# Kernel optimization log

Hardware: AMD Instinct MI355X
Metric: run time of the kernel (lower is better)

## Reference

```python
import jax, jax.numpy as jnp
import numpy as np

KS, STRIDE, PAD, GROUPS = 7, 1, 3, 8


def setup_inputs() -> dict:
    key = jax.random.key(0)
    ks = jax.random.split(key, 6)
    B, C, H, W = 4, 128, 64, 64
    O = 128
    rel_size = O // GROUPS // 2  # 8
    return {
        "x": jax.random.normal(ks[0], (B, C, H, W), jnp.float32),
        "wq": jax.random.normal(ks[1], (O, C), jnp.float32) * 0.05,
        "wk": jax.random.normal(ks[2], (O, C), jnp.float32) * 0.05,
        "wv": jax.random.normal(ks[3], (O, C), jnp.float32) * 0.05,
        "rel_x": jax.random.normal(ks[4], (rel_size, KS), jnp.float32),
        "rel_y": jax.random.normal(ks[5], (O // GROUPS - rel_size, KS), jnp.float32),
    }


def _patches(a, fH, fW):
    # a: [B, C, pH, pW] -> [B, C, fH, fW, KS, KS] (overlapping windows, like torch unfold)
    cols = []
    for ki in range(KS):
        rows = []
        for kj in range(KS):
            rows.append(a[:, :, ki:ki + (fH - 1) * STRIDE + 1:STRIDE,
                             kj:kj + (fW - 1) * STRIDE + 1:STRIDE])
        cols.append(jnp.stack(rows, axis=-1))  # last axis = l (W-kernel)
    return jnp.stack(cols, axis=-2)            # second-to-last = k (H-kernel)


def reference(x, wq, wk, wv, rel_x, rel_y):
    B, C, H, W = x.shape
    O = wq.shape[0]
    rel_size = rel_x.shape[0]
    xp = jnp.pad(x, ((0, 0), (0, 0), (PAD, PAD), (PAD, PAD)))
    pH, pW = H + 2 * PAD, W + 2 * PAD
    fH, fW = (pH - KS) // STRIDE + 1, (pW - KS) // STRIDE + 1
    # 1x1 convs
    q = jnp.einsum('oc,bchw->bohw', wq, xp)
    k = jnp.einsum('oc,bchw->bohw', wk, xp)
    v = jnp.einsum('oc,bchw->bohw', wv, xp)
    h0 = (KS - 1) // 2
    win_q = q[:, :, h0:pH - KS // 2:STRIDE, h0:pW - KS // 2:STRIDE]  # [B,O,fH,fW]
    win_q_b = win_q.reshape(B, GROUPS, O // GROUPS, fH, fW)
    qx = win_q_b[:, :, :rel_size]
    qy = win_q_b[:, :, rel_size:]
    bias_x = jnp.einsum('bgxhw,xk->bhwk', qx, rel_x)  # varies along l (W-kernel)
    bias_y = jnp.einsum('bgyhw,yk->bhwk', qy, rel_y)  # varies along k (H-kernel)
    win_k = _patches(k, fH, fW)  # [B,O,fH,fW,KS,KS]
    win_v = _patches(v, fH, fW)
    logits = jnp.einsum('bchw,bchwkl->bhwkl', win_q, win_k)
    logits = logits + bias_x[:, :, :, None, :] + bias_y[:, :, :, :, None]
    attn = jax.nn.softmax(logits.reshape(B, fH, fW, KS * KS), axis=-1)
    attn = attn.reshape(B, fH, fW, KS, KS)
    out = jnp.einsum('bhwkl,bchwkl->bchw', attn, win_v)  # [B,O,fH,fW]
    return out
```

## Files before the change

### kernel.cpp

```cpp
#include <hip/hip_runtime.h>

typedef __fp16 half8_t __attribute__((ext_vector_type(8)));
typedef float  f4_t    __attribute__((ext_vector_type(4)));

__device__ __forceinline__ unsigned pk(float a, float b) {
    return __builtin_bit_cast(unsigned, __builtin_amdgcn_cvt_pkrtz(a, b));
}

__global__ __launch_bounds__(256, 4) void qkv_fused(
    const float* __restrict__ x, const float* __restrict__ wq,
    const float* __restrict__ wk, const float* __restrict__ wv,
    const float* __restrict__ relx, const float* __restrict__ rely,
    unsigned* __restrict__ qf, unsigned* __restrict__ kf,
    unsigned* __restrict__ vf, float* __restrict__ biasG)
{
    __shared__ __fp16 Af[2048 * 8];
    __shared__ float  uB[4][320];
    __shared__ float  relsQ[120];

    const int tid = threadIdx.x, wvn = tid >> 6, lane = tid & 63;
    const int mtx = blockIdx.x >> 8;
    const int tg  = blockIdx.x & 255;
    const float* wsrc = (mtx == 0) ? wq : (mtx == 1 ? wk : wv);
    unsigned*    dst  = (mtx == 0) ? qf : (mtx == 1 ? kf : vf);

    if (tid < 120)
        relsQ[tid] = (tid < 56) ? relx[tid] : (tid < 112 ? rely[tid - 56] : 0.f);

#pragma unroll
    for (int s = 0; s < 8; ++s) {
        const int it = s * 256 + tid;
        const int l = it & 63, ck = (it >> 6) & 3, ot = it >> 8;
        const float* wr = wsrc + (size_t)(ot * 16 + (l & 15)) * 128 + ck * 32 + (l >> 4) * 8;
        const float4 w0 = *(const float4*)wr;
        const float4 w1 = *(const float4*)(wr + 4);
        unsigned* d = (unsigned*)&Af[it * 8];
        d[0] = pk(w0.x, w0.y); d[1] = pk(w0.z, w0.w);
        d[2] = pk(w1.x, w1.y); d[3] = pk(w1.z, w1.w);
    }

    const int t = tg * 4 + wvn;
    const int m = lane & 15, quad = lane >> 4;
    const int p0 = t * 16, b = p0 >> 12, hw = p0 & 4095;
    const float* xb = x + (size_t)b * (128 * 4096) + hw + m;
    half8_t B[4];
#pragma unroll
    for (int ck = 0; ck < 4; ++ck) {
        float f[8];
#pragma unroll
        for (int j = 0; j < 8; ++j) f[j] = xb[(size_t)(ck * 32 + quad * 8 + j) * 4096];
        unsigned* d = (unsigned*)&B[ck];
        d[0] = pk(f[0], f[1]); d[1] = pk(f[2], f[3]);
        d[2] = pk(f[4], f[5]); d[3] = pk(f[6], f[7]);
    }
    __syncthreads();

    float* tl = uB[wvn];
    float s0 = 0.f, s1 = 0.f, s2 = 0.f, s3 = 0.f;
#pragma unroll
    for (int og = 0; og < 4; ++og) {
#pragma unroll
        for (int ot = 0; ot < 2; ++ot) {
            const int otile = og * 2 + ot;
            f4_t acc = {0.f, 0.f, 0.f, 0.f};
#pragma unroll
            for (int ck = 0; ck < 4; ++ck) {
                const half8_t A = *(const half8_t*)&Af[((otile * 4 + ck) * 64 + lane) * 8];
                acc = __builtin_amdgcn_mfma_f32_16x16x32_f16(A, B[ck], acc, 0, 0, 0);
            }
            if (mtx == 0) { s0 += acc[0]; s1 += acc[1]; s2 += acc[2]; s3 += acc[3]; }
            const int c2l = ot * 8 + quad * 2;
            tl[m * 17 + c2l]     = __builtin_bit_cast(float, pk(acc[0], acc[1]));
            tl[m * 17 + c2l + 1] = __builtin_bit_cast(float, pk(acc[2], acc[3]));
        }
        __asm__ volatile("s_waitcnt lgkmcnt(0)" ::: "memory");
        __builtin_amdgcn_wave_barrier();
#pragma unroll
        for (int s = 0; s < 4; ++s) {
            const int px = s * 4 + quad;
            dst[(size_t)(p0 + px) * 64 + og * 16 + m] =
                __builtin_bit_cast(unsigned, tl[px * 17 + m]);
        }
        __builtin_amdgcn_wave_barrier();
    }

    if (mtx == 0) {
        float* sS = uB[wvn];
        f4_t sv = {s0, s1, s2, s3};
        __asm__ volatile("s_waitcnt lgkmcnt(0)" ::: "memory");
        __builtin_amdgcn_wave_barrier();
        *(f4_t*)&sS[m * 20 + quad * 4] = sv;
        __asm__ volatile("s_waitcnt lgkmcnt(0)" ::: "memory");
        __builtin_amdgcn_wave_barrier();
        f4_t bj = {0.f, 0.f, 0.f, 0.f};
#pragma unroll
        for (int jj = 0; jj < 4; ++jj) {
            const int j = quad * 4 + jj;
            float s = 0.f;
            if (j < 7) {
#pragma unroll
                for (int tt = 0; tt < 8; ++tt)
                    s = fmaf(sS[m * 20 + tt], relsQ[tt * 7 + j], s);
            } else if (j < 14) {
#pragma unroll
                for (int tt = 0; tt < 8; ++tt)
                    s = fmaf(sS[m * 20 + 8 + tt], relsQ[56 + tt * 7 + (j - 7)], s);
            }
            bj[jj] = s;
        }
        *(f4_t*)(biasG + (size_t)(p0 + m) * 16 + quad * 4) = bj;
    }
}

constexpr int VP = 168;

__global__ __launch_bounds__(256) void attn_mfma(
    const unsigned* __restrict__ qf, const unsigned* __restrict__ kf,
    const unsigned* __restrict__ vf, const float* __restrict__ biasG,
    float* __restrict__ out)
{
    __shared__ __fp16 vH[128 * VP];
    __shared__ __fp16 aW[2][16 * 136];
    __shared__ float  biasL[32 * 16];

    const int tid = threadIdx.x, bx = blockIdx.x;
    const int wv = tid >> 6, lane = tid & 63;
    const int w0 = (bx & 7) * 8;
    const int h0 = ((bx >> 3) & 15) * 4;
    const int b  = bx >> 7;
    const int s  = wv >> 1, u = wv & 1;
    const int wr = h0 + 2 * s + u;
    const int n16 = lane & 15, quad = lane >> 4;

    for (int i = tid; i < 2176; i += 256) ((unsigned*)aW)[i] = 0u;

    {
        const int g = tid >> 3, r = tid & 7;
#pragma unroll
        for (int it = 0; it < 5; ++it) {
            const int pq = r + 8 * it;
            const int hi = pq >> 2, ciq = pq & 3;
            const int py = h0 - 3 + hi;
            unsigned d0[4], d1[4];
#pragma unroll
            for (int p = 0; p < 4; ++p) {
                const int pxc = w0 - 3 + ciq * 4 + p;
                uint2 d = make_uint2(0u, 0u);
                if ((unsigned)py < 64u && (unsigned)pxc < 64u)
                    d = *(const uint2*)(vf + (size_t)((b * 4096 + py * 64 + pxc) * 64 + g * 2));
                d0[p] = d.x; d1[p] = d.y;
            }
            const int c0 = g * 4, off = hi * 16 + ciq * 4;
            *(uint2*)(vH + (c0 + 0) * VP + off) = make_uint2(
                __builtin_amdgcn_perm(d0[1], d0[0], 0x05040100u),
                __builtin_amdgcn_perm(d0[3], d0[2], 0x05040100u));
            *(uint2*)(vH + (c0 + 1) * VP + off) = make_uint2(
                __builtin_amdgcn_perm(d0[1], d0[0], 0x07060302u),
                __builtin_amdgcn_perm(d0[3], d0[2], 0x07060302u));
            *(uint2*)(vH + (c0 + 2) * VP + off) = make_uint2(
                __builtin_amdgcn_perm(d1[1], d1[0], 0x05040100u),
                __builtin_amdgcn_perm(d1[3], d1[2], 0x05040100u));
            *(uint2*)(vH + (c0 + 3) * VP + off) = make_uint2(
                __builtin_amdgcn_perm(d1[1], d1[0], 0x07060302u),
                __builtin_amdgcn_perm(d1[3], d1[2], 0x07060302u));
        }
    }

    for (int i = tid; i < 512; i += 256) {
        const int px = i >> 4, tt = i & 15;
        const int pix = b * 4096 + (h0 + (px >> 3)) * 64 + w0 + (px & 7);
        biasL[px * 16 + tt] = biasG[(size_t)pix * 16 + tt];
    }
    __syncthreads();

    uint4 qA[4];
    {
        const bool vm = n16 < 8;
        const size_t qb = (size_t)(b * 4096 + wr * 64 + w0 + n16) * 64;
#pragma unroll
        for (int kc = 0; kc < 4; ++kc) {
            uint4 t4 = make_uint4(0u, 0u, 0u, 0u);
            if (vm) t4 = *(const uint4*)(qf + qb + kc * 16 + quad * 4);
            qA[kc] = t4;
        }
    }
    f4_t lg[7];
#pragma unroll
    for (int t = 0; t < 7; ++t) {
        const int py = wr - 3 + t;
        const int pxc = w0 - 3 + n16;
        const bool val = ((unsigned)py < 64u) && ((unsigned)pxc < 64u);
        const size_t kb = (size_t)(b * 4096 + py * 64 + pxc) * 64;
        f4_t acc = {0.f, 0.f, 0.f, 0.f};
#pragma unroll
        for (int kc = 0; kc < 4; ++kc) {
            uint4 kB = make_uint4(0u, 0u, 0u, 0u);
            if (val) kB = *(const uint4*)(kf + kb + kc * 16 + quad * 4);
            acc = __builtin_amdgcn_mfma_f32_16x16x32_f16(
                __builtin_bit_cast(half8_t, qA[kc]),
                __builtin_bit_cast(half8_t, kB), acc, 0, 0, 0);
        }
        lg[t] = acc;
    }

    const int rowblk = 2 * s + u;
#pragma unroll
    for (int i = 0; i < 4; ++i) {
        const int m = quad * 4 + i;
        const float* bb = &biasL[(rowblk * 8 + (m & 7)) * 16];
        const int kj = n16 - m;
        const bool kv = (unsigned)kj < 7u;
        const float bx2 = kv ? bb[kj] : 0.f;
        float lv[7];
        float mx = -1e30f;
#pragma unroll
        for (int t = 0; t < 7; ++t) {
            const float v = kv ? lg[t][i] + bx2 + bb[7 + t] : -1e30f;
            lv[t] = v;
            mx = fmaxf(mx, v);
        }
        mx = fmaxf(mx, __shfl_xor(mx, 1));
        mx = fmaxf(mx, __shfl_xor(mx, 2));
        mx = fmaxf(mx, __shfl_xor(mx, 4));
        mx = fmaxf(mx, __shfl_xor(mx, 8));
        float ss = 0.f;
#pragma unroll
        for (int t = 0; t < 7; ++t) {
            const float e = __expf(lv[t] - mx);
            lv[t] = e;
            ss += e;
        }
        ss += __shfl_xor(ss, 1);
        ss += __shfl_xor(ss, 2);
        ss += __shfl_xor(ss, 4);
        ss += __shfl_xor(ss, 8);
        const float inv = 1.f / ss;
        if (m < 8) {
            __fp16* wp = &aW[s][(u * 8 + m) * 136];
#pragma unroll
            for (int t = 0; t < 7; ++t)
                wp[(u + t) * 16 + n16] = (__fp16)(lv[t] * inv);
        }
    }
    __syncthreads();

    uint4 pA[4];
#pragma unroll
    for (int kc = 0; kc < 4; ++kc)
        pA[kc] = *(const uint4*)(&aW[s][n16 * 136 + kc * 32 + quad * 8]);
#pragma unroll
    for (int tt = 0; tt < 4; ++tt) {
        const int tn = u * 4 + tt;
        f4_t acc = {0.f, 0.f, 0.f, 0.f};
#pragma unroll
        for (int kc = 0; kc < 4; ++kc) {
            const int kri = kc * 2 + (quad >> 1);
            const int ci0 = (quad & 1) * 8;
            const half8_t vB = *(const half8_t*)(
                vH + (tn * 16 + n16) * VP + (2 * s + kri) * 16 + ci0);
            acc = __builtin_amdgcn_mfma_f32_16x16x32_f16(
                __builtin_bit_cast(half8_t, pA[kc]), vB, acc, 0, 0, 0);
        }
        const int c = tn * 16 + n16;
        float* ob = out + (size_t)(b * 128 + c) * 4096;
#pragma unroll
        for (int i = 0; i < 4; ++i) {
            const int mm = quad * 4 + i;
            ob[(h0 + 2 * s + (mm >> 3)) * 64 + w0 + (mm & 7)] = acc[i];
        }
    }
}

extern "C" void kernel_launch(void* const* d_in, const int* in_sizes, int n_in,
                              void* d_out, int out_size, void* d_ws, size_t ws_size,
                              hipStream_t stream) {
    const float* x    = (const float*)d_in[0];
    const float* wq   = (const float*)d_in[1];
    const float* wk   = (const float*)d_in[2];
    const float* wv   = (const float*)d_in[3];
    const float* relx = (const float*)d_in[4];
    const float* rely = (const float*)d_in[5];
    float* out = (float*)d_out;

    char* ws = (char*)d_ws;
    unsigned* qfb = (unsigned*)(ws);
    unsigned* kfb = (unsigned*)(ws + 0x400000);
    unsigned* vfb = (unsigned*)(ws + 0x800000);
    float*    bG  = (float*)   (ws + 0xC00000);

    qkv_fused<<<dim3(768), 256, 0, stream>>>(x, wq, wk, wv, relx, rely,
                                             qfb, kfb, vfb, bG);
    attn_mfma<<<dim3(512), 256, 0, stream>>>(qfb, kfb, vfb, bG, out);
}
```

Measured before the change: 98.50 us.

## Load QKV weights directly into registers and store MFMA output without LDS staging

```diff
diff --git a/kernel.cpp b/kernel.cpp
--- a/kernel.cpp
+++ b/kernel.cpp
@@ -7,16 +7,15 @@
     return __builtin_bit_cast(unsigned, __builtin_amdgcn_cvt_pkrtz(a, b));
 }
 
-__global__ __launch_bounds__(256, 4) void qkv_fused(
+__global__ __launch_bounds__(256) void qkv_direct(
     const float* __restrict__ x, const float* __restrict__ wq,
     const float* __restrict__ wk, const float* __restrict__ wv,
     const float* __restrict__ relx, const float* __restrict__ rely,
     unsigned* __restrict__ qf, unsigned* __restrict__ kf,
     unsigned* __restrict__ vf, float* __restrict__ biasG)
 {
-    __shared__ __fp16 Af[2048 * 8];
-    __shared__ float  uB[4][320];
-    __shared__ float  relsQ[120];
+    __shared__ float sS[4][320];
+    __shared__ float relsQ[120];
 
     const int tid = threadIdx.x, wvn = tid >> 6, lane = tid & 63;
     const int mtx = blockIdx.x >> 8;
@@ -24,23 +23,12 @@
     const float* wsrc = (mtx == 0) ? wq : (mtx == 1 ? wk : wv);
     unsigned*    dst  = (mtx == 0) ? qf : (mtx == 1 ? kf : vf);
 
-    if (tid < 120)
+    if (mtx == 0 && tid < 120)
         relsQ[tid] = (tid < 56) ? relx[tid] : (tid < 112 ? rely[tid - 56] : 0.f);
 
-#pragma unroll
-    for (int s = 0; s < 8; ++s) {
-        const int it = s * 256 + tid;
-        const int l = it & 63, ck = (it >> 6) & 3, ot = it >> 8;
-        const float* wr = wsrc + (size_t)(ot * 16 + (l & 15)) * 128 + ck * 32 + (l >> 4) * 8;
-        const float4 w0 = *(const float4*)wr;
-        const float4 w1 = *(const float4*)(wr + 4);
-        unsigned* d = (unsigned*)&Af[it * 8];
-        d[0] = pk(w0.x, w0.y); d[1] = pk(w0.z, w0.w);
-        d[2] = pk(w1.x, w1.y); d[3] = pk(w1.z, w1.w);
-    }
+    const int m = lane & 15, quad = lane >> 4;
 
     const int t = tg * 4 + wvn;
-    const int m = lane & 15, quad = lane >> 4;
     const int p0 = t * 16, b = p0 >> 12, hw = p0 & 4095;
     const float* xb = x + (size_t)b * (128 * 4096) + hw + m;
     half8_t B[4];
@@ -53,43 +41,33 @@
         d[0] = pk(f[0], f[1]); d[1] = pk(f[2], f[3]);
         d[2] = pk(f[4], f[5]); d[3] = pk(f[6], f[7]);
     }
-    __syncthreads();
-
-    float* tl = uB[wvn];
+
     float s0 = 0.f, s1 = 0.f, s2 = 0.f, s3 = 0.f;
-#pragma unroll
-    for (int og = 0; og < 4; ++og) {
-#pragma unroll
-        for (int ot = 0; ot < 2; ++ot) {
-            const int otile = og * 2 + ot;
-            f4_t acc = {0.f, 0.f, 0.f, 0.f};
-#pragma unroll
-            for (int ck = 0; ck < 4; ++ck) {
-                const half8_t A = *(const half8_t*)&Af[((otile * 4 + ck) * 64 + lane) * 8];
-                acc = __builtin_amdgcn_mfma_f32_16x16x32_f16(A, B[ck], acc, 0, 0, 0);
-            }
-            if (mtx == 0) { s0 += acc[0]; s1 += acc[1]; s2 += acc[2]; s3 += acc[3]; }
-            const int c2l = ot * 8 + quad * 2;
-            tl[m * 17 + c2l]     = __builtin_bit_cast(float, pk(acc[0], acc[1]));
-            tl[m * 17 + c2l + 1] = __builtin_bit_cast(float, pk(acc[2], acc[3]));
-        }
-        __asm__ volatile("s_waitcnt lgkmcnt(0)" ::: "memory");
-        __builtin_amdgcn_wave_barrier();
-#pragma unroll
-        for (int s = 0; s < 4; ++s) {
-            const int px = s * 4 + quad;
-            dst[(size_t)(p0 + px) * 64 + og * 16 + m] =
-                __builtin_bit_cast(unsigned, tl[px * 17 + m]);
-        }
-        __builtin_amdgcn_wave_barrier();
+    unsigned* dpx = dst + (size_t)(p0 + m) * 64 + quad * 2;
+#pragma unroll
+    for (int og = 0; og < 8; ++og) {
+        half8_t A[4];
+#pragma unroll
+        for (int kc = 0; kc < 4; ++kc) {
+            const float* wr = wsrc + (size_t)(og * 16 + m) * 128 + kc * 32 + quad * 8;
+            const float4 w0 = *(const float4*)wr;
+            const float4 w1 = *(const float4*)(wr + 4);
+            unsigned* d = (unsigned*)&A[kc];
+            d[0] = pk(w0.x, w0.y); d[1] = pk(w0.z, w0.w);
+            d[2] = pk(w1.x, w1.y); d[3] = pk(w1.z, w1.w);
+        }
+        f4_t acc = {0.f, 0.f, 0.f, 0.f};
+#pragma unroll
+        for (int kc = 0; kc < 4; ++kc)
+            acc = __builtin_amdgcn_mfma_f32_16x16x32_f16(A[kc], B[kc], acc, 0, 0, 0);
+        if (mtx == 0) { s0 += acc[0]; s1 += acc[1]; s2 += acc[2]; s3 += acc[3]; }
+        *(uint2*)(dpx + og * 8) = make_uint2(pk(acc[0], acc[1]), pk(acc[2], acc[3]));
     }
 
     if (mtx == 0) {
-        float* sS = uB[wvn];
-        f4_t sv = {s0, s1, s2, s3};
-        __asm__ volatile("s_waitcnt lgkmcnt(0)" ::: "memory");
-        __builtin_amdgcn_wave_barrier();
-        *(f4_t*)&sS[m * 20 + quad * 4] = sv;
+        __syncthreads();
+        float* sw = sS[wvn];
+        *(f4_t*)&sw[m * 20 + quad * 4] = (f4_t){s0, s1, s2, s3};
         __asm__ volatile("s_waitcnt lgkmcnt(0)" ::: "memory");
         __builtin_amdgcn_wave_barrier();
         f4_t bj = {0.f, 0.f, 0.f, 0.f};
@@ -100,11 +78,11 @@
             if (j < 7) {
 #pragma unroll
                 for (int tt = 0; tt < 8; ++tt)
-                    s = fmaf(sS[m * 20 + tt], relsQ[tt * 7 + j], s);
+                    s = fmaf(sw[m * 20 + tt], relsQ[tt * 7 + j], s);
             } else if (j < 14) {
 #pragma unroll
                 for (int tt = 0; tt < 8; ++tt)
-                    s = fmaf(sS[m * 20 + 8 + tt], relsQ[56 + tt * 7 + (j - 7)], s);
+                    s = fmaf(sw[m * 20 + 8 + tt], relsQ[56 + tt * 7 + (j - 7)], s);
             }
             bj[jj] = s;
         }
@@ -288,7 +266,7 @@
     unsigned* vfb = (unsigned*)(ws + 0x800000);
     float*    bG  = (float*)   (ws + 0xC00000);
 
-    qkv_fused<<<dim3(768), 256, 0, stream>>>(x, wq, wk, wv, relx, rely,
-                                             qfb, kfb, vfb, bG);
+    qkv_direct<<<dim3(768), 256, 0, stream>>>(x, wq, wk, wv, relx, rely,
+                                              qfb, kfb, vfb, bG);
     attn_mfma<<<dim3(512), 256, 0, stream>>>(qfb, kfb, vfb, bG, out);
 }
```

Measured after the change: 113.6 us. 15.3% more time.
